# Optimization experiments

Measured on AMD Instinct MI355X. Metric: run time of the kernel, lower is better.

Reference implementation:

```python
import jax, jax.numpy as jnp
import numpy as np
from jax import lax

WBITS = 4
BN_EPS = 1e-5


def quantize_weight_symmetric(w, wbits=WBITS):
    # Per-tensor symmetric uniform quantization with straight-through estimator.
    qmax = float(2 ** (wbits - 1) - 1)  # 7 for 4-bit
    scale = jnp.max(jnp.abs(w)) / qmax
    wq = jnp.clip(jnp.round(w / scale), -qmax, qmax) * scale
    # STE: forward uses wq, backward passes gradient straight through to w
    return w + lax.stop_gradient(wq - w)


def setup_inputs() -> dict:
    key = jax.random.key(0)
    k1, k2 = jax.random.split(key)
    x = jax.random.normal(k1, (32, 128, 56, 56), dtype=jnp.float32)
    w = jax.random.normal(k2, (256, 128, 3, 3), dtype=jnp.float32) * 0.05
    gamma = jnp.ones((256,), dtype=jnp.float32)
    beta = jnp.zeros((256,), dtype=jnp.float32)
    return {"x": x, "w": w, "gamma": gamma, "beta": beta}


def reference(x, w, gamma, beta):
    # Quantized conv (QConv, bias=False, stride=1, padding=1)
    wq = quantize_weight_symmetric(w)
    out = lax.conv_general_dilated(
        x, wq,
        window_strides=(1, 1),
        padding=[(1, 1), (1, 1)],
        dimension_numbers=("NCHW", "OIHW", "NCHW"),
    )  # [N, 256, 56, 56]
    # BatchNorm2d in training mode: batch statistics over (N, H, W)
    mean = jnp.mean(out, axis=(0, 2, 3))
    var = jnp.var(out, axis=(0, 2, 3))
    inv = gamma * lax.rsqrt(var + BN_EPS)
    out = out * inv[None, :, None, None] + (beta - mean * inv)[None, :, None, None]
    # abits=32 -> full-precision activation (ReLU)
    return jax.nn.relu(out)
```

## Files before the change

kernel.cpp:

```cpp
#include <hip/hip_runtime.h>

typedef unsigned short u16;
typedef unsigned int u32;
typedef __attribute__((ext_vector_type(4))) float f32x4;
typedef __attribute__((ext_vector_type(8))) short short8;

#define HWD 56
#define HW2 3136
#define C_IN 128
#define K_OUT 256
#define N_IMG 32
#define CHW_IN 401408
#define CHW_OUT 802816
#define PIX 100352
#define WQ_N 294912
#define GROWS 1872
#define XROW 1856
#define XPLANE (GROWS * XROW)
#define NR 10
#define BCHUNKS 2320
#define BPITCH 40
#define BELEMS 23200
#define NSLICE 1568
#define CV_OFF 33554432u
#define WS_NEED_BF16 (CV_OFF + (size_t)PIX * K_OUT * 2)

__device__ __forceinline__ u16 f2bf(float f) {
    u32 u = __float_as_uint(f);
    u32 r = u + 0x7FFFu + ((u >> 16) & 1u);
    return (u16)(r >> 16);
}

__device__ __forceinline__ void glds16(const u16* g, u16* l) {
    __builtin_amdgcn_global_load_lds(
        (const __attribute__((address_space(1))) void*)g,
        (__attribute__((address_space(3))) void*)l, 16, 0, 0);
}

__global__ void maxabs_k(const float* __restrict__ w, u32* __restrict__ wsmax) {
    float m = 0.f;
    for (int i = blockIdx.x * blockDim.x + threadIdx.x; i < WQ_N; i += gridDim.x * blockDim.x)
        m = fmaxf(m, fabsf(w[i]));
    for (int off = 32; off; off >>= 1)
        m = fmaxf(m, __shfl_xor(m, off));
    __shared__ float sm[4];
    int lane = threadIdx.x & 63, wid = threadIdx.x >> 6;
    if (lane == 0) sm[wid] = m;
    __syncthreads();
    if (threadIdx.x == 0) {
        float mm = fmaxf(fmaxf(sm[0], sm[1]), fmaxf(sm[2], sm[3]));
        atomicMax(wsmax, __float_as_uint(mm));
    }
}

__global__ void quant_t_k5(const float* __restrict__ w, const u32* __restrict__ wsmax,
                           u16* __restrict__ wqt) {
    int o = blockIdx.x * 256 + threadIdx.x;
    if (o >= WQ_N) return;
    int j = o & 7;
    int mrow = (o >> 3) & 127;
    int oct = (o >> 10) & 3;
    int mt = (o >> 12) & 1;
    int kt = o >> 13;
    int cq = kt / 9, tap = kt - cq * 9;
    int c = cq * 32 + oct * 8 + j;
    int m = mt * 128 + mrow;
    float scale = __uint_as_float(wsmax[0]) / 7.0f;
    float q = rintf(w[(m * 128 + c) * 9 + tap] / scale);
    q = fminf(fmaxf(q, -7.0f), 7.0f);
    wqt[o] = f2bf(q * scale);
}

__global__ void halo_zero(u16* __restrict__ xt3) {
    int i = blockIdx.x * 256 + threadIdx.x;
    u32 addr;
    if (i < 74240) {
        int rowIdx = i / 928, rem = i - rowIdx * 928;
        int cq = rem / 232, c = rem - cq * 232;
        int row = rowIdx < 64 ? (rowIdx >> 1) * 58 + (rowIdx & 1) * 57 : 1856 + (rowIdx - 64);
        addr = (u32)cq * XPLANE + row * XROW + c * 8;
    } else {
        int j = i - 74240;
        int rowd = j >> 5, rem = j & 31;
        int side = rem >> 4, cq = (rem >> 2) & 3, o4 = rem & 3;
        int n = rowd / 56, h = rowd - n * 56;
        int row = n * 58 + 1 + h, col = side * 57;
        addr = (u32)cq * XPLANE + (row * 58 + col) * 32 + o4 * 8;
    }
    *(uint4*)(xt3 + addr) = (uint4){0, 0, 0, 0};
}

__global__ __launch_bounds__(256) void pad_transpose(const float* __restrict__ x,
                                                     u16* __restrict__ xt3) {
    __shared__ float T[128][57];
    const int tid = threadIdx.x;
    const int n = blockIdx.x / HWD;
    const int h = blockIdx.x - n * HWD;
    const float* srow = x + (size_t)n * CHW_IN + h * HWD;
    #pragma unroll
    for (int it = 0; it < 7; ++it) {
        int i = tid + it * 256;
        int c = i / 14, q = i - c * 14;
        float4 v = *(const float4*)(srow + c * HW2 + q * 4);
        T[c][q * 4 + 0] = v.x; T[c][q * 4 + 1] = v.y;
        T[c][q * 4 + 2] = v.z; T[c][q * 4 + 3] = v.w;
    }
    __syncthreads();
    const int gRow = n * 58 + 1 + h;
    #pragma unroll
    for (int it = 0; it < 4; ++it) {
        int i = tid + it * 256;
        if (i < 56 * 16) {
            int w = i >> 4, oc = i & 15;
            int cq = oc >> 2, o4 = oc & 3;
            union { u16 us[8]; uint4 v4; } pk;
            #pragma unroll
            for (int j = 0; j < 8; ++j) pk.us[j] = f2bf(T[oc * 8 + j][w]);
            *(uint4*)(xt3 + (size_t)cq * XPLANE + (gRow * 58 + (w + 1)) * 32 + o4 * 8) = pk.v4;
        }
    }
}

template <bool BF16OUT>
__global__ __launch_bounds__(256, 2) void conv_m(const u16* __restrict__ xt3,
                                                 const u16* __restrict__ wqt,
                                                 float* __restrict__ out,
                                                 u16* __restrict__ cvout,
                                                 float* __restrict__ P) {
    __shared__ __align__(16) u16 lds[35488];
    const int tid = threadIdx.x;
    const int lane = tid & 63;
    const int w4 = tid >> 6;
    const int fr = lane & 15, fq = lane >> 4;
    const int swz = (blockIdx.x & 7) * 98 + (blockIdx.x >> 3);
    const int nt = swz >> 1, mt = swz & 1;
    const int p0 = nt * 256;
    const int R0 = (p0 / HW2) * 58 + (p0 % HW2) / HWD;

    int bElem[4];
    #pragma unroll
    for (int ni = 0; ni < 4; ++ni) {
        int px = p0 + w4 * 64 + ni * 16 + fr;
        int img = px / HW2, hw = px - img * HW2;
        int gr = img * 58 + 1 + hw / HWD;
        int pixLin = (gr - R0) * 58 + (hw % HWD) + 1;
        bElem[ni] = (pixLin - 59) * BPITCH + fq * 8;
    }

#define ABUF(b) (&lds[BELEMS + (b) * 4096])
#define STAGE_A(kt_, b_) do {                                              \
        const u16* ga_ = wqt + (size_t)(((kt_) * 2 + mt)) * 4096;          \
        glds16(ga_ + tid * 8,         ABUF(b_) + tid * 8);                 \
        glds16(ga_ + (tid + 256) * 8, ABUF(b_) + (tid + 256) * 8);         \
    } while (0)
#define GATE2() asm volatile("s_waitcnt vmcnt(2)" ::: "memory")
#define GATE0() asm volatile("s_waitcnt vmcnt(0)" ::: "memory")
#define BAR() __builtin_amdgcn_s_barrier()

    f32x4 acc[8][4];
    #pragma unroll
    for (int a = 0; a < 8; ++a)
        #pragma unroll
        for (int b = 0; b < 4; ++b)
            acc[a][b] = (f32x4){0.f, 0.f, 0.f, 0.f};

    STAGE_A(0, 0);
    STAGE_A(1, 1);

    #pragma unroll 1
    for (int cq = 0; cq < 4; ++cq) {
        {
            const u16* bsrc = xt3 + (size_t)cq * XPLANE + (size_t)R0 * XROW;
            uint4 breg[10];
            #pragma unroll
            for (int i = 0; i < 10; ++i) {
                int c = tid + i * 256;
                if (c < BCHUNKS) breg[i] = *(const uint4*)(bsrc + c * 8);
            }
            GATE0();
            #pragma unroll
            for (int i = 0; i < 10; ++i) {
                int c = tid + i * 256;
                if (c < BCHUNKS)
                    *(uint4*)&lds[(c >> 2) * BPITCH + (c & 3) * 8] = breg[i];
            }
        }
        __syncthreads();

        #pragma unroll
        for (int it = 0; it < 3; ++it) {
            #pragma unroll
            for (int u = 0; u < 3; ++u) {
                const int tt = it * 3 + u;
                const int kt = cq * 9 + tt;
                if (kt + 2 < 36) STAGE_A(kt + 2, (tt + 2) % 3);
                short8 pf[4], wf[4];
                #pragma unroll
                for (int ni = 0; ni < 4; ++ni)
                    pf[ni] = *(const short8*)&lds[bElem[ni] + (it * 58 + u) * BPITCH];
                #pragma unroll
                for (int mi = 0; mi < 4; ++mi)
                    wf[mi] = *(const short8*)&(ABUF(tt % 3)[fq * 1024 + mi * 128 + fr * 8]);
                __builtin_amdgcn_s_setprio(1);
                #pragma unroll
                for (int mi = 0; mi < 4; ++mi)
                    #pragma unroll
                    for (int ni = 0; ni < 4; ++ni)
                        acc[mi][ni] = __builtin_amdgcn_mfma_f32_16x16x32_bf16(
                            pf[ni], wf[mi], acc[mi][ni], 0, 0, 0);
                __builtin_amdgcn_s_setprio(0);
                #pragma unroll
                for (int mi = 0; mi < 4; ++mi)
                    wf[mi] = *(const short8*)&(ABUF(tt % 3)[fq * 1024 + (mi + 4) * 128 + fr * 8]);
                __builtin_amdgcn_s_setprio(1);
                #pragma unroll
                for (int mi = 0; mi < 4; ++mi)
                    #pragma unroll
                    for (int ni = 0; ni < 4; ++ni)
                        acc[mi + 4][ni] = __builtin_amdgcn_mfma_f32_16x16x32_bf16(
                            pf[ni], wf[mi], acc[mi + 4][ni], 0, 0, 0);
                __builtin_amdgcn_s_setprio(0);
                if (kt < 34) GATE2();
                else if (kt == 34) GATE0();
                BAR();
            }
        }
    }

    const int slice = nt * 4 + w4;
    #pragma unroll
    for (int mi = 0; mi < 8; ++mi) {
        float s = 0.f, q = 0.f;
        #pragma unroll
        for (int ni = 0; ni < 4; ++ni)
            #pragma unroll
            for (int j = 0; j < 4; ++j) {
                float v = acc[mi][ni][j];
                s += v; q += v * v;
            }
        s += __shfl_xor(s, 16); s += __shfl_xor(s, 32);
        q += __shfl_xor(q, 16); q += __shfl_xor(q, 32);
        if (fq == 0) {
            int ch = mt * 128 + mi * 16 + fr;
            float* dst = P + ((size_t)ch * NSLICE + slice) * 2;
            dst[0] = s; dst[1] = q;
        }
    }

    if (BF16OUT) {
        u16* T = lds;
        #pragma unroll
        for (int p = 0; p < 2; ++p) {
            __syncthreads();
            #pragma unroll
            for (int c2 = 0; c2 < 4; ++c2) {
                const int lch = c2 * 16 + fr;
                #pragma unroll
                for (int ni = 0; ni < 4; ++ni) {
                    union { u16 h[4]; uint2 v; } pk;
                    #pragma unroll
                    for (int j = 0; j < 4; ++j) pk.h[j] = f2bf(acc[p * 4 + c2][ni][j]);
                    *(uint2*)&T[lch * 264 + w4 * 64 + ni * 16 + fq * 4] = pk.v;
                }
            }
            __syncthreads();
            #pragma unroll
            for (int i = 0; i < 8; ++i) {
                int q = tid + i * 256;
                int lch = q >> 5, pxc = q & 31;
                uint4 v = *(const uint4*)&T[lch * 264 + pxc * 8];
                int ch = mt * 128 + p * 64 + lch;
                *(uint4*)&cvout[(size_t)ch * PIX + p0 + pxc * 8] = v;
            }
        }
    } else {
        #pragma unroll
        for (int mi = 0; mi < 8; ++mi) {
            int ch = mt * 128 + mi * 16 + fr;
            #pragma unroll
            for (int ni = 0; ni < 4; ++ni)
                #pragma unroll
                for (int j = 0; j < 4; ++j) {
                    int px = p0 + w4 * 64 + ni * 16 + fq * 4 + j;
                    int n = px / HW2, hw = px - n * HW2;
                    out[(size_t)n * CHW_OUT + (size_t)ch * HW2 + hw] = acc[mi][ni][j];
                }
        }
    }
#undef ABUF
#undef STAGE_A
#undef GATE2
#undef GATE0
#undef BAR
}

__global__ void stats_fin(const float* __restrict__ P, const float* __restrict__ gamma,
                          const float* __restrict__ beta, float* __restrict__ stats) {
    int ch = blockIdx.x;
    int tid = threadIdx.x;
    float s = 0.f, q = 0.f;
    const float* base = P + (size_t)ch * NSLICE * 2;
    for (int i = tid; i < NSLICE; i += 256) {
        float2 v = *(const float2*)(base + i * 2);
        s += v.x; q += v.y;
    }
    for (int m = 32; m; m >>= 1) { s += __shfl_xor(s, m); q += __shfl_xor(q, m); }
    __shared__ float ss[4], qs[4];
    int l = tid & 63, w = tid >> 6;
    if (l == 0) { ss[w] = s; qs[w] = q; }
    __syncthreads();
    if (tid == 0) {
        float S = ss[0] + ss[1] + ss[2] + ss[3];
        float Q = qs[0] + qs[1] + qs[2] + qs[3];
        float mean = S / (float)PIX;
        float var = Q / (float)PIX - mean * mean;
        float inv = gamma[ch] * rsqrtf(var + 1e-5f);
        stats[2 * ch] = inv;
        stats[2 * ch + 1] = beta[ch] - mean * inv;
    }
}

__global__ void bn_relu_nchw(const u16* __restrict__ cvout, float* __restrict__ out,
                             const float* __restrict__ stats) {
    const int b = blockIdx.x;
    const int ch = b / 49, g = b - ch * 49;
    const float inv = stats[2 * ch], sh = stats[2 * ch + 1];
    const int p8 = (g * 256 + threadIdx.x) * 8;
    short8 v = *(const short8*)&cvout[(size_t)ch * PIX + p8];
    const int n = p8 / HW2;
    const int hw = p8 - n * HW2;
    float* dst = out + ((size_t)n * K_OUT + ch) * HW2 + hw;
    f32x4 o0, o1;
    #pragma unroll
    for (int j = 0; j < 4; ++j) {
        float a = __uint_as_float(((u32)(u16)v[j]) << 16);
        float bb = __uint_as_float(((u32)(u16)v[j + 4]) << 16);
        o0[j] = fmaxf(a * inv + sh, 0.f);
        o1[j] = fmaxf(bb * inv + sh, 0.f);
    }
    *(f32x4*)dst = o0;
    *(f32x4*)(dst + 4) = o1;
}

__global__ void bn_relu_f32(float* __restrict__ out, const float* __restrict__ stats) {
    const int n4 = ((size_t)N_IMG * K_OUT * HW2) / 4;
    int stride = gridDim.x * blockDim.x;
    for (int i = blockIdx.x * blockDim.x + threadIdx.x; i < n4; i += stride) {
        int ch = (i / (HW2 / 4)) & (K_OUT - 1);
        float inv = stats[2 * ch], sh = stats[2 * ch + 1];
        f32x4 v = ((f32x4*)out)[i];
        #pragma unroll
        for (int j = 0; j < 4; ++j)
            v[j] = fmaxf(v[j] * inv + sh, 0.f);
        ((f32x4*)out)[i] = v;
    }
}

extern "C" void kernel_launch(void* const* d_in, const int* in_sizes, int n_in,
                              void* d_out, int out_size, void* d_ws, size_t ws_size,
                              hipStream_t stream) {
    const float* x = (const float*)d_in[0];
    const float* w = (const float*)d_in[1];
    const float* gamma = (const float*)d_in[2];
    const float* beta = (const float*)d_in[3];
    float* out = (float*)d_out;

    char* ws = (char*)d_ws;
    u32* wsmax = (u32*)ws;
    float* stats = (float*)(ws + 64);
    u16* wqt = (u16*)(ws + 4096);
    float* P = (float*)(ws + 1048576u);
    u16* xt3 = (u16*)(ws + 4325376u);
    u16* cvout = (u16*)(ws + CV_OFF);
    const bool bf16path = (ws_size >= WS_NEED_BF16);

    hipMemsetAsync(wsmax, 0, 64, stream);
    maxabs_k<<<128, 256, 0, stream>>>(w, wsmax);
    quant_t_k5<<<WQ_N / 256, 256, 0, stream>>>(w, wsmax, wqt);
    halo_zero<<<514, 256, 0, stream>>>(xt3);
    pad_transpose<<<N_IMG * HWD, 256, 0, stream>>>(x, xt3);
    if (bf16path) {
        conv_m<true><<<784, 256, 0, stream>>>(xt3, wqt, out, cvout, P);
        stats_fin<<<K_OUT, 256, 0, stream>>>(P, gamma, beta, stats);
        bn_relu_nchw<<<K_OUT * 49, 256, 0, stream>>>(cvout, out, stats);
    } else {
        conv_m<false><<<784, 256, 0, stream>>>(xt3, wqt, out, cvout, P);
        stats_fin<<<K_OUT, 256, 0, stream>>>(P, gamma, beta, stats);
        bn_relu_f32<<<4096, 256, 0, stream>>>(out, stats);
    }
}
```

Measured before the change: 146.3 us.

## Load conv operands directly from global memory instead of LDS staging

The conv kernel stops staging the activation tile and the weight tiles in shared memory, which used async global-to-LDS copies, triple buffering and a barrier per tap. Each wave now reads its MFMA fragments straight from global memory (the padded NHWC-ish activation layout and the pre-transposed weights) and relies on the caches for reuse. This removes the LDS fills, waitcnt gates and barriers, and shrinks LDS to the output-transpose buffer. In exchange it adds many more global/cache loads per MFMA with no explicit prefetching, so the loads may be exposed as latency.

New measurement: 170.4 us. 16.5% more time.

```diff
diff --git a/kernel.cpp b/kernel.cpp
--- a/kernel.cpp
+++ b/kernel.cpp
@@ -17,10 +17,6 @@
 #define GROWS 1872
 #define XROW 1856
 #define XPLANE (GROWS * XROW)
-#define NR 10
-#define BCHUNKS 2320
-#define BPITCH 40
-#define BELEMS 23200
 #define NSLICE 1568
 #define CV_OFF 33554432u
 #define WS_NEED_BF16 (CV_OFF + (size_t)PIX * K_OUT * 2)
@@ -29,12 +25,6 @@
     u32 u = __float_as_uint(f);
     u32 r = u + 0x7FFFu + ((u >> 16) & 1u);
     return (u16)(r >> 16);
-}
-
-__device__ __forceinline__ void glds16(const u16* g, u16* l) {
-    __builtin_amdgcn_global_load_lds(
-        (const __attribute__((address_space(1))) void*)g,
-        (__attribute__((address_space(3))) void*)l, 16, 0, 0);
 }
 
 __global__ void maxabs_k(const float* __restrict__ w, u32* __restrict__ wsmax) {
@@ -122,12 +112,12 @@
 }
 
 template <bool BF16OUT>
-__global__ __launch_bounds__(256, 2) void conv_m(const u16* __restrict__ xt3,
-                                                 const u16* __restrict__ wqt,
-                                                 float* __restrict__ out,
-                                                 u16* __restrict__ cvout,
-                                                 float* __restrict__ P) {
-    __shared__ __align__(16) u16 lds[35488];
+__global__ __launch_bounds__(256, 2) void conv_df(const u16* __restrict__ xt3,
+                                                  const u16* __restrict__ wqt,
+                                                  float* __restrict__ out,
+                                                  u16* __restrict__ cvout,
+                                                  float* __restrict__ P) {
+    __shared__ __align__(16) u16 T[16896];
     const int tid = threadIdx.x;
     const int lane = tid & 63;
     const int w4 = tid >> 6;
@@ -135,27 +125,17 @@
     const int swz = (blockIdx.x & 7) * 98 + (blockIdx.x >> 3);
     const int nt = swz >> 1, mt = swz & 1;
     const int p0 = nt * 256;
-    const int R0 = (p0 / HW2) * 58 + (p0 % HW2) / HWD;
-
-    int bElem[4];
+
+    int bG[4];
     #pragma unroll
     for (int ni = 0; ni < 4; ++ni) {
         int px = p0 + w4 * 64 + ni * 16 + fr;
         int img = px / HW2, hw = px - img * HW2;
-        int gr = img * 58 + 1 + hw / HWD;
-        int pixLin = (gr - R0) * 58 + (hw % HWD) + 1;
-        bElem[ni] = (pixLin - 59) * BPITCH + fq * 8;
-    }
-
-#define ABUF(b) (&lds[BELEMS + (b) * 4096])
-#define STAGE_A(kt_, b_) do {                                              \
-        const u16* ga_ = wqt + (size_t)(((kt_) * 2 + mt)) * 4096;          \
-        glds16(ga_ + tid * 8,         ABUF(b_) + tid * 8);                 \
-        glds16(ga_ + (tid + 256) * 8, ABUF(b_) + (tid + 256) * 8);         \
-    } while (0)
-#define GATE2() asm volatile("s_waitcnt vmcnt(2)" ::: "memory")
-#define GATE0() asm volatile("s_waitcnt vmcnt(0)" ::: "memory")
-#define BAR() __builtin_amdgcn_s_barrier()
+        int g = img * 58 + 1 + hw / HWD;
+        int wc = hw % HWD + 1;
+        bG[ni] = ((g - 1) * 58 + (wc - 1)) * 32 + fq * 8;
+    }
+    const int aOff = fq * 1024 + fr * 8;
 
     f32x4 acc[8][4];
     #pragma unroll
@@ -164,66 +144,37 @@
         for (int b = 0; b < 4; ++b)
             acc[a][b] = (f32x4){0.f, 0.f, 0.f, 0.f};
 
-    STAGE_A(0, 0);
-    STAGE_A(1, 1);
-
     #pragma unroll 1
     for (int cq = 0; cq < 4; ++cq) {
-        {
-            const u16* bsrc = xt3 + (size_t)cq * XPLANE + (size_t)R0 * XROW;
-            uint4 breg[10];
-            #pragma unroll
-            for (int i = 0; i < 10; ++i) {
-                int c = tid + i * 256;
-                if (c < BCHUNKS) breg[i] = *(const uint4*)(bsrc + c * 8);
-            }
-            GATE0();
-            #pragma unroll
-            for (int i = 0; i < 10; ++i) {
-                int c = tid + i * 256;
-                if (c < BCHUNKS)
-                    *(uint4*)&lds[(c >> 2) * BPITCH + (c & 3) * 8] = breg[i];
-            }
-        }
-        __syncthreads();
-
-        #pragma unroll
-        for (int it = 0; it < 3; ++it) {
-            #pragma unroll
-            for (int u = 0; u < 3; ++u) {
-                const int tt = it * 3 + u;
-                const int kt = cq * 9 + tt;
-                if (kt + 2 < 36) STAGE_A(kt + 2, (tt + 2) % 3);
-                short8 pf[4], wf[4];
+        const u16* bP = xt3 + (size_t)cq * XPLANE;
+        #pragma unroll
+        for (int tap = 0; tap < 9; ++tap) {
+            const int kt = cq * 9 + tap;
+            const int r = tap / 3, s = tap - r * 3;
+            const int toff = (r * 58 + s) * 32;
+            const u16* aK = wqt + (size_t)(kt * 2 + mt) * 4096;
+            short8 pf[4], wf[4];
+            #pragma unroll
+            for (int ni = 0; ni < 4; ++ni)
+                pf[ni] = *(const short8*)(bP + bG[ni] + toff);
+            #pragma unroll
+            for (int mi = 0; mi < 4; ++mi)
+                wf[mi] = *(const short8*)(aK + aOff + mi * 128);
+            #pragma unroll
+            for (int mi = 0; mi < 4; ++mi)
                 #pragma unroll
                 for (int ni = 0; ni < 4; ++ni)
-                    pf[ni] = *(const short8*)&lds[bElem[ni] + (it * 58 + u) * BPITCH];
+                    acc[mi][ni] = __builtin_amdgcn_mfma_f32_16x16x32_bf16(
+                        pf[ni], wf[mi], acc[mi][ni], 0, 0, 0);
+            #pragma unroll
+            for (int mi = 0; mi < 4; ++mi)
+                wf[mi] = *(const short8*)(aK + aOff + (mi + 4) * 128);
+            #pragma unroll
+            for (int mi = 0; mi < 4; ++mi)
                 #pragma unroll
-                for (int mi = 0; mi < 4; ++mi)
-                    wf[mi] = *(const short8*)&(ABUF(tt % 3)[fq * 1024 + mi * 128 + fr * 8]);
-                __builtin_amdgcn_s_setprio(1);
-                #pragma unroll
-                for (int mi = 0; mi < 4; ++mi)
-                    #pragma unroll
-                    for (int ni = 0; ni < 4; ++ni)
-                        acc[mi][ni] = __builtin_amdgcn_mfma_f32_16x16x32_bf16(
-                            pf[ni], wf[mi], acc[mi][ni], 0, 0, 0);
-                __builtin_amdgcn_s_setprio(0);
-                #pragma unroll
-                for (int mi = 0; mi < 4; ++mi)
-                    wf[mi] = *(const short8*)&(ABUF(tt % 3)[fq * 1024 + (mi + 4) * 128 + fr * 8]);
-                __builtin_amdgcn_s_setprio(1);
-                #pragma unroll
-                for (int mi = 0; mi < 4; ++mi)
-                    #pragma unroll
-                    for (int ni = 0; ni < 4; ++ni)
-                        acc[mi + 4][ni] = __builtin_amdgcn_mfma_f32_16x16x32_bf16(
-                            pf[ni], wf[mi], acc[mi + 4][ni], 0, 0, 0);
-                __builtin_amdgcn_s_setprio(0);
-                if (kt < 34) GATE2();
-                else if (kt == 34) GATE0();
-                BAR();
-            }
+                for (int ni = 0; ni < 4; ++ni)
+                    acc[mi + 4][ni] = __builtin_amdgcn_mfma_f32_16x16x32_bf16(
+                        pf[ni], wf[mi], acc[mi + 4][ni], 0, 0, 0);
         }
     }
 
@@ -248,7 +199,6 @@
     }
 
     if (BF16OUT) {
-        u16* T = lds;
         #pragma unroll
         for (int p = 0; p < 2; ++p) {
             __syncthreads();
@@ -287,11 +237,6 @@
                 }
         }
     }
-#undef ABUF
-#undef STAGE_A
-#undef GATE2
-#undef GATE0
-#undef BAR
 }
 
 __global__ void stats_fin(const float* __restrict__ P, const float* __restrict__ gamma,
@@ -380,11 +325,11 @@
     halo_zero<<<514, 256, 0, stream>>>(xt3);
     pad_transpose<<<N_IMG * HWD, 256, 0, stream>>>(x, xt3);
     if (bf16path) {
-        conv_m<true><<<784, 256, 0, stream>>>(xt3, wqt, out, cvout, P);
+        conv_df<true><<<784, 256, 0, stream>>>(xt3, wqt, out, cvout, P);
         stats_fin<<<K_OUT, 256, 0, stream>>>(P, gamma, beta, stats);
         bn_relu_nchw<<<K_OUT * 49, 256, 0, stream>>>(cvout, out, stats);
     } else {
-        conv_m<false><<<784, 256, 0, stream>>>(xt3, wqt, out, cvout, P);
+        conv_df<false><<<784, 256, 0, stream>>>(xt3, wqt, out, cvout, P);
         stats_fin<<<K_OUT, 256, 0, stream>>>(P, gamma, beta, stats);
         bn_relu_f32<<<4096, 256, 0, stream>>>(out, stats);
     }
```
